# Kernel tuning notes

Hardware: AMD Instinct MI355X
Metric: run time of the kernel (lower is better)

Reference implementation:

```python
import jax, jax.numpy as jnp
import numpy as np

B, T, E = 4, 2_000_000, 8
C, K, STRIDE = 128, 512, 512
CHUNK, OVERLAP = 64000, 511  # overlap defaults to kernel_size - 1


def _candidate_positions(T):
    """Exact set of window start positions visited by the chunked streaming max.

    Replays the chunk loop of _lowmem_max_over_time: chunk starts advance by
    step = chunk_size - overlap (not a multiple of stride!), and within each
    chunk conv windows start at chunk_start + stride*k.
    """
    step = max(1, CHUNK - OVERLAP)
    pos = []
    start = 0
    while start < T:
        end = min(start + CHUNK, T)
        end_ext = min(end + OVERLAP, T)
        L = end_ext - start
        if L >= K:
            n = (L - K) // STRIDE + 1
            pos.append(start + STRIDE * np.arange(n, dtype=np.int64))
        if end == T:
            break
        start += step
    p = np.unique(np.concatenate(pos))
    return np.clip(p, 0, max(0, T - K))


POS = _candidate_positions(T)                       # [P] static window starts
WIN_IDX = POS[:, None] + np.arange(K, dtype=np.int64)  # [P, K] gather indices


def setup_inputs() -> dict:
    key = jax.random.key(0)
    ks = jax.random.split(key, 5)
    scale = 1.0 / float(np.sqrt(E * K))  # torch Conv1d default init range
    return {
        "x": jax.random.normal(ks[0], (B, T, E), dtype=jnp.float32),
        "w1": jax.random.uniform(ks[1], (C, E, K), jnp.float32, -scale, scale),
        "b1": jax.random.uniform(ks[2], (C,), jnp.float32, -scale, scale),
        "w2": jax.random.uniform(ks[3], (C, E, K), jnp.float32, -scale, scale),
        "b2": jax.random.uniform(ks[4], (C,), jnp.float32, -scale, scale),
    }


def reference(x, w1, b1, w2, b2):
    # Gather every candidate window the chunked scan would see: [B, P, K, E]
    wins = x[:, WIN_IDX, :]
    # Original clones windows under no_grad (stop_grad_input=True): input gets no grad.
    wins = jax.lax.stop_gradient(wins)
    # Gated conv (GLU): conv1(z) * sigmoid(conv2(z)) at each window -> [B, C, P]
    c1 = jnp.einsum('bpke,cek->bcp', wins, w1) + b1[:, None]
    c2 = jnp.einsum('bpke,cek->bcp', wins, w2) + b2[:, None]
    g = c1 * jax.nn.sigmoid(c2)
    # Global max-over-time per (batch, channel); identical value to the
    # running-max pass followed by exact re-evaluation at argmax positions.
    return g.max(axis=-1)  # [B, C]
```

## Files before the change

### kernel.cpp

```cpp
#include <hip/hip_runtime.h>


#define T_LEN 2000000
#define P_CNT 3937
#define M_TOT 15748
#define KD    4096

typedef __attribute__((ext_vector_type(8))) short short8;
typedef __attribute__((ext_vector_type(4))) float f32x4;

static __device__ __forceinline__ unsigned short f2bf(float f) {
    unsigned u = __builtin_bit_cast(unsigned, f);
    unsigned r = (u + 0x7FFFu + ((u >> 16) & 1u)) >> 16;
    return (unsigned short)r;
}

static __device__ __forceinline__ unsigned ordenc(float f) {
    unsigned u = __builtin_bit_cast(unsigned, f);
    return (u & 0x80000000u) ? ~u : (u | 0x80000000u);
}

static __device__ __forceinline__ size_t row_base_bp(int bb, int p) {
    int j, kp;
    if (p < 3875) { j = p / 125; kp = p - j * 125; }
    else          { j = 31;      kp = p - 3875; }
    long pos = (long)j * 63489 + (long)kp * 512;
    return ((size_t)bb * T_LEN + (size_t)pos) * 8u;
}

static __device__ __forceinline__ uint2 cvt4(float4 v) {
    unsigned lo, hi;
    asm("v_cvt_pk_bf16_f32 %0, %1, %2" : "=v"(lo) : "v"(v.x), "v"(v.y));
    asm("v_cvt_pk_bf16_f32 %0, %1, %2" : "=v"(hi) : "v"(v.z), "v"(v.w));
    uint2 u; u.x = lo; u.y = hi;
    return u;
}

__global__ __launch_bounds__(256) void pack_w(const float* __restrict__ w1,
                                              const float* __restrict__ w2,
                                              uint4* __restrict__ Bpf,
                                              unsigned* __restrict__ outu) {
    int c = blockIdx.x * 256 + threadIdx.x;
    if (c < 512) outu[c] = 0u;
    if (c >= 131072) return;
    int l  = c & 63;
    int g  = (c >> 6) & 7;
    int nf = (c >> 9) & 1;
    int kq = (c >> 10) & 1;
    int ks = c >> 11;
    int n  = nf ? (128 + g * 16 + (l & 15)) : (g * 16 + (l & 15));
    int kb = ks * 64 + kq * 32 + ((l >> 4) << 3);
    const float* src = (n < 128) ? w1 : w2;
    int cc = n & 127;
    unsigned short h[8];
#pragma unroll
    for (int j = 0; j < 8; ++j) {
        int k = kb + j;
        h[j] = f2bf(src[cc * 4096 + (k & 7) * 512 + (k >> 3)]);
    }
    uint4 v;
    v.x = (unsigned)h[0] | ((unsigned)h[1] << 16);
    v.y = (unsigned)h[2] | ((unsigned)h[3] << 16);
    v.z = (unsigned)h[4] | ((unsigned)h[5] << 16);
    v.w = (unsigned)h[6] | ((unsigned)h[7] << 16);
    Bpf[c] = v;
}

#define LOAD_B(BB, KS)                                                         \
    do {                                                                       \
        _Pragma("unroll")                                                      \
        for (int kq = 0; kq < 2; ++kq)                                         \
            _Pragma("unroll")                                                  \
            for (int nf = 0; nf < 2; ++nf)                                     \
                BB[kq][nf] = Bq[((KS) * 4 + kq * 2 + nf) * 512 + bbase];       \
    } while (0)

#define STEP_NB(KS, BCUR, BNXT)                                                \
    do {                                                                       \
        const int ks_ = (KS);                                                  \
        const int ksn = (ks_ + 1 < 64) ? ks_ + 1 : 63;                         \
        LOAD_B(BNXT, ksn);                                                     \
        const int ksl = (ks_ + 6 < 64) ? ks_ + 6 : 63;                         \
        float4 aF = *(const float4*)(x + aoff + (size_t)(ksl * 64));           \
        const char* As = smem + (ks_ & 7) * 4096;                              \
        _Pragma("unroll")                                                      \
        for (int kq = 0; kq < 2; ++kq) {                                       \
            short8 af0 = *(const short8*)(As + aro[kq][0]);                    \
            short8 af1 = *(const short8*)(As + aro[kq][1]);                    \
            short8 b0  = __builtin_bit_cast(short8, BCUR[kq][0]);              \
            short8 b1  = __builtin_bit_cast(short8, BCUR[kq][1]);              \
            acc[0][0] = __builtin_amdgcn_mfma_f32_16x16x32_bf16(               \
                af0, b0, acc[0][0], 0, 0, 0);                                  \
            acc[1][0] = __builtin_amdgcn_mfma_f32_16x16x32_bf16(               \
                af1, b0, acc[1][0], 0, 0, 0);                                  \
            acc[0][1] = __builtin_amdgcn_mfma_f32_16x16x32_bf16(               \
                af0, b1, acc[0][1], 0, 0, 0);                                  \
            acc[1][1] = __builtin_amdgcn_mfma_f32_16x16x32_bf16(               \
                af1, b1, acc[1][1], 0, 0, 0);                                  \
        }                                                                      \
        if (ks_ + 4 < 64)                                                      \
            *(uint2*)(smem + ((ks_ + 4) & 7) * 4096 + awb) = cvt4(aA);         \
        aA = aB; aB = aF;                                                      \
    } while (0)

__global__ __launch_bounds__(512, 4) void gemm_max(const float* __restrict__ x,
                                                   const uint4* __restrict__ Bq,
                                                   const float* __restrict__ b1,
                                                   const float* __restrict__ b2,
                                                   unsigned* __restrict__ outu) {
    __shared__ __align__(16) char smem[32768];

    const int t    = threadIdx.x;
    const int lane = t & 63;
    const int g    = t >> 6;
    const int bid  = blockIdx.x;
    const int bb   = bid / 124;
    const int p0   = (bid % 124) * 32;

    const int rowS = t >> 4;
    const int kcS  = t & 15;
    int pS = p0 + rowS; if (pS > P_CNT - 1) pS = P_CNT - 1;
    const size_t aoff = row_base_bp(bb, pS) + (size_t)(kcS * 4);
    const int    awb  = (rowS * 128 + kcS * 8) ^ ((rowS & 7) << 4);

    int aro[2][2];
#pragma unroll
    for (int kq = 0; kq < 2; ++kq)
#pragma unroll
        for (int mf = 0; mf < 2; ++mf) {
            int row = mf * 16 + (lane & 15);
            aro[kq][mf] = (row * 128 + kq * 64 + (lane >> 4) * 16)
                          ^ ((row & 7) << 4);
        }

    const int bbase = g * 64 + lane;

#pragma unroll
    for (int pt = 0; pt < 4; ++pt) {
        float4 v = *(const float4*)(x + aoff + pt * 64);
        *(uint2*)(smem + pt * 4096 + awb) = cvt4(v);
    }
    __syncthreads();

    float4 aA = *(const float4*)(x + aoff + 256);
    float4 aB = *(const float4*)(x + aoff + 320);
    uint4 BX[2][2], BY[2][2];
    LOAD_B(BX, 0);

    f32x4 acc[2][2];
#pragma unroll
    for (int mf = 0; mf < 2; ++mf)
#pragma unroll
        for (int nf = 0; nf < 2; ++nf) acc[mf][nf] = (f32x4){0.f, 0.f, 0.f, 0.f};

    for (int ks = 0; ks < 64; ks += 2) {
        STEP_NB(ks, BX, BY);
        STEP_NB(ks + 1, BY, BX);
        asm volatile("s_waitcnt lgkmcnt(14)" ::: "memory");
        __builtin_amdgcn_s_barrier();
        asm volatile("" ::: "memory");
    }

    const int   cidx = g * 16 + (lane & 15);
    const float bb1  = b1[cidx];
    const float bb2  = b2[cidx];
    float best = -3.4e38f;
#pragma unroll
    for (int mf = 0; mf < 2; ++mf)
#pragma unroll
        for (int q = 0; q < 4; ++q) {
            float c1 = acc[mf][0][q] + bb1;
            float c2 = acc[mf][1][q] + bb2;
            float gv = c1 / (1.f + __expf(-c2));
            best = fmaxf(best, gv);
        }
    best = fmaxf(best, __shfl_xor(best, 16));
    best = fmaxf(best, __shfl_xor(best, 32));
    if (lane < 16)
        atomicMax(&outu[bb * 128 + cidx], ordenc(best));
}

__global__ __launch_bounds__(256) void unmap_out(unsigned* __restrict__ outu) {
    int i = blockIdx.x * 256 + threadIdx.x;
    if (i < 512) {
        unsigned u = outu[i];
        outu[i] = (u & 0x80000000u) ? (u ^ 0x80000000u) : ~u;
    }
}

extern "C" void kernel_launch(void* const* d_in, const int* in_sizes, int n_in,
                              void* d_out, int out_size, void* d_ws, size_t ws_size,
                              hipStream_t stream) {
    const float* x  = (const float*)d_in[0];
    const float* w1 = (const float*)d_in[1];
    const float* b1 = (const float*)d_in[2];
    const float* w2 = (const float*)d_in[3];
    const float* b2 = (const float*)d_in[4];

    uint4*    Bpf  = (uint4*)d_ws;
    unsigned* outu = (unsigned*)d_out;

    pack_w<<<dim3(512), dim3(256), 0, stream>>>(w1, w2, Bpf, outu);

    const int nblk = 124 * 4;
    gemm_max<<<dim3(nblk), dim3(512), 0, stream>>>(x, (const uint4*)Bpf, b1, b2, outu);

    unmap_out<<<dim3(2), dim3(256), 0, stream>>>(outu);
}
```

Before: 87.45 us.

## Double the M tile per block to 64 rows to reuse B fragments

Each block now handles 64 window rows instead of 32, with 4 M-fragments per wave. Every loaded B fragment therefore feeds twice as many MFMAs, and the grid halves to 248 blocks. Each thread stages 8 elements with wider LDS writes, and LDS grows to 64KB. The risks are fewer blocks than the MI355X has CUs (256), which lowers parallelism, plus higher register and LDS pressure that may reduce occupancy.

```diff
diff --git a/kernel.cpp b/kernel.cpp
--- a/kernel.cpp
+++ b/kernel.cpp
@@ -81,26 +81,28 @@
         const int ksn = (ks_ + 1 < 64) ? ks_ + 1 : 63;                         \
         LOAD_B(BNXT, ksn);                                                     \
         const int ksl = (ks_ + 6 < 64) ? ks_ + 6 : 63;                         \
-        float4 aF = *(const float4*)(x + aoff + (size_t)(ksl * 64));           \
-        const char* As = smem + (ks_ & 7) * 4096;                              \
+        float4 aF0 = *(const float4*)(x + aoff + (size_t)(ksl * 64));          \
+        float4 aF1 = *(const float4*)(x + aoff + (size_t)(ksl * 64) + 4);      \
+        const char* As = smem + (ks_ & 7) * 8192;                              \
         _Pragma("unroll")                                                      \
         for (int kq = 0; kq < 2; ++kq) {                                       \
-            short8 af0 = *(const short8*)(As + aro[kq][0]);                    \
-            short8 af1 = *(const short8*)(As + aro[kq][1]);                    \
-            short8 b0  = __builtin_bit_cast(short8, BCUR[kq][0]);              \
-            short8 b1  = __builtin_bit_cast(short8, BCUR[kq][1]);              \
-            acc[0][0] = __builtin_amdgcn_mfma_f32_16x16x32_bf16(               \
-                af0, b0, acc[0][0], 0, 0, 0);                                  \
-            acc[1][0] = __builtin_amdgcn_mfma_f32_16x16x32_bf16(               \
-                af1, b0, acc[1][0], 0, 0, 0);                                  \
-            acc[0][1] = __builtin_amdgcn_mfma_f32_16x16x32_bf16(               \
-                af0, b1, acc[0][1], 0, 0, 0);                                  \
-            acc[1][1] = __builtin_amdgcn_mfma_f32_16x16x32_bf16(               \
-                af1, b1, acc[1][1], 0, 0, 0);                                  \
+            short8 b0 = __builtin_bit_cast(short8, BCUR[kq][0]);               \
+            short8 b1 = __builtin_bit_cast(short8, BCUR[kq][1]);               \
+            _Pragma("unroll")                                                  \
+            for (int mf = 0; mf < 4; ++mf) {                                   \
+                short8 af = *(const short8*)(As + aro[kq][mf]);                \
+                acc[mf][0] = __builtin_amdgcn_mfma_f32_16x16x32_bf16(          \
+                    af, b0, acc[mf][0], 0, 0, 0);                              \
+                acc[mf][1] = __builtin_amdgcn_mfma_f32_16x16x32_bf16(          \
+                    af, b1, acc[mf][1], 0, 0, 0);                              \
+            }                                                                  \
         }                                                                      \
-        if (ks_ + 4 < 64)                                                      \
-            *(uint2*)(smem + ((ks_ + 4) & 7) * 4096 + awb) = cvt4(aA);         \
-        aA = aB; aB = aF;                                                      \
+        if (ks_ + 4 < 64) {                                                    \
+            uint2 lo = cvt4(aA0), hi = cvt4(aA1);                              \
+            uint4 wv; wv.x = lo.x; wv.y = lo.y; wv.z = hi.x; wv.w = hi.y;      \
+            *(uint4*)(smem + ((ks_ + 4) & 7) * 8192 + awb) = wv;               \
+        }                                                                      \
+        aA0 = aB0; aA1 = aB1; aB0 = aF0; aB1 = aF1;                            \
     } while (0)
 
 __global__ __launch_bounds__(512, 4) void gemm_max(const float* __restrict__ x,
@@ -108,26 +110,25 @@
                                                    const float* __restrict__ b1,
                                                    const float* __restrict__ b2,
                                                    unsigned* __restrict__ outu) {
-    __shared__ __align__(16) char smem[32768];
+    __shared__ __align__(16) char smem[65536];
 
     const int t    = threadIdx.x;
     const int lane = t & 63;
     const int g    = t >> 6;
     const int bid  = blockIdx.x;
-    const int bb   = bid / 124;
-    const int p0   = (bid % 124) * 32;
-
-    const int rowS = t >> 4;
-    const int kcS  = t & 15;
+    const int bb   = bid / 62;
+    const int p0   = (bid % 62) * 64;
+
+    const int rowS = t >> 3;
     int pS = p0 + rowS; if (pS > P_CNT - 1) pS = P_CNT - 1;
-    const size_t aoff = row_base_bp(bb, pS) + (size_t)(kcS * 4);
-    const int    awb  = (rowS * 128 + kcS * 8) ^ ((rowS & 7) << 4);
-
-    int aro[2][2];
+    const size_t aoff = row_base_bp(bb, pS) + (size_t)((t & 7) * 8);
+    const int    awb  = (rowS * 128 + (t & 7) * 16) ^ ((rowS & 7) << 4);
+
+    int aro[2][4];
 #pragma unroll
     for (int kq = 0; kq < 2; ++kq)
 #pragma unroll
-        for (int mf = 0; mf < 2; ++mf) {
+        for (int mf = 0; mf < 4; ++mf) {
             int row = mf * 16 + (lane & 15);
             aro[kq][mf] = (row * 128 + kq * 64 + (lane >> 4) * 16)
                           ^ ((row & 7) << 4);
@@ -137,26 +138,31 @@
 
 #pragma unroll
     for (int pt = 0; pt < 4; ++pt) {
-        float4 v = *(const float4*)(x + aoff + pt * 64);
-        *(uint2*)(smem + pt * 4096 + awb) = cvt4(v);
+        float4 v0 = *(const float4*)(x + aoff + pt * 64);
+        float4 v1 = *(const float4*)(x + aoff + pt * 64 + 4);
+        uint2 lo = cvt4(v0), hi = cvt4(v1);
+        uint4 wv; wv.x = lo.x; wv.y = lo.y; wv.z = hi.x; wv.w = hi.y;
+        *(uint4*)(smem + pt * 8192 + awb) = wv;
     }
     __syncthreads();
 
-    float4 aA = *(const float4*)(x + aoff + 256);
-    float4 aB = *(const float4*)(x + aoff + 320);
+    float4 aA0 = *(const float4*)(x + aoff + 256);
+    float4 aA1 = *(const float4*)(x + aoff + 260);
+    float4 aB0 = *(const float4*)(x + aoff + 320);
+    float4 aB1 = *(const float4*)(x + aoff + 324);
     uint4 BX[2][2], BY[2][2];
     LOAD_B(BX, 0);
 
-    f32x4 acc[2][2];
-#pragma unroll
-    for (int mf = 0; mf < 2; ++mf)
+    f32x4 acc[4][2];
+#pragma unroll
+    for (int mf = 0; mf < 4; ++mf)
 #pragma unroll
         for (int nf = 0; nf < 2; ++nf) acc[mf][nf] = (f32x4){0.f, 0.f, 0.f, 0.f};
 
     for (int ks = 0; ks < 64; ks += 2) {
         STEP_NB(ks, BX, BY);
         STEP_NB(ks + 1, BY, BX);
-        asm volatile("s_waitcnt lgkmcnt(14)" ::: "memory");
+        asm volatile("s_waitcnt lgkmcnt(15)" ::: "memory");
         __builtin_amdgcn_s_barrier();
         asm volatile("" ::: "memory");
     }
@@ -166,7 +172,7 @@
     const float bb2  = b2[cidx];
     float best = -3.4e38f;
 #pragma unroll
-    for (int mf = 0; mf < 2; ++mf)
+    for (int mf = 0; mf < 4; ++mf)
 #pragma unroll
         for (int q = 0; q < 4; ++q) {
             float c1 = acc[mf][0][q] + bb1;
@@ -202,7 +208,7 @@
 
     pack_w<<<dim3(512), dim3(256), 0, stream>>>(w1, w2, Bpf, outu);
 
-    const int nblk = 124 * 4;
+    const int nblk = 62 * 4;
     gemm_max<<<dim3(nblk), dim3(512), 0, stream>>>(x, (const uint4*)Bpf, b1, b2, outu);
 
     unmap_out<<<dim3(2), dim3(256), 0, stream>>>(outu);
```

After: 73.18 us. 1.2x faster.
